# Performance work log

Measured on AMD Instinct MI355X. Metric: run time of the kernel, lower is better.

## Reference

```python
import jax, jax.numpy as jnp
import numpy as np

D_MODEL = 256
NUM_HEADS = 8
HEAD_DIM = D_MODEL // NUM_HEADS


def setup_inputs() -> dict:
    key = jax.random.key(0)
    ks = jax.random.split(key, 16)
    B, C, H, W = 2, D_MODEL, 64, 64
    s = 0.02
    inp = {
        "query_feat": jax.random.normal(ks[0], (B, C, H, W), jnp.float32),
        "lateral_feat": jax.random.normal(ks[1], (B, C, H, W), jnp.float32),
        # 1x1 convs == per-pixel linear layers: weight (out, in), bias (out,)
        "Wq": jax.random.normal(ks[2], (C, C), jnp.float32) * s,
        "bq": jnp.zeros((C,), jnp.float32),
        "Wk": jax.random.normal(ks[3], (C, C), jnp.float32) * s,
        "bk": jnp.zeros((C,), jnp.float32),
        "Wv": jax.random.normal(ks[4], (C, C), jnp.float32) * s,
        "bv": jnp.zeros((C,), jnp.float32),
        "Wo": jax.random.normal(ks[5], (C, C), jnp.float32) * s,
        "bo": jnp.zeros((C,), jnp.float32),
        "W1": jax.random.normal(ks[6], (4 * C, C), jnp.float32) * s,
        "b1": jnp.zeros((4 * C,), jnp.float32),
        "W2": jax.random.normal(ks[7], (C, 4 * C), jnp.float32) * s,
        "b2": jnp.zeros((C,), jnp.float32),
    }
    return inp


def reference(query_feat, lateral_feat, Wq, bq, Wk, bk, Wv, bv, Wo, bo, W1, b1, W2, b2):
    B, C, H, W = query_feat.shape
    N = H * W
    h, d = NUM_HEADS, HEAD_DIM
    scale = d ** -0.5

    # (B,C,H,W) -> (B,N,C) tokens
    xq = query_feat.reshape(B, C, N).transpose(0, 2, 1)
    xl = lateral_feat.reshape(B, C, N).transpose(0, 2, 1)

    # 1x1-conv projections = dense per-token linear
    Q = (xq @ Wq.T + bq).reshape(B, N, h, d).transpose(0, 2, 1, 3)  # (B,h,N,d)
    K = (xl @ Wk.T + bk).reshape(B, N, h, d).transpose(0, 2, 1, 3)
    V = (xl @ Wv.T + bv).reshape(B, N, h, d).transpose(0, 2, 1, 3)

    scores = jnp.einsum("bhqd,bhkd->bhqk", Q, K) * scale  # (B,h,N,N)
    attn = jax.nn.softmax(scores, axis=-1)  # dropout = identity at inference
    out = jnp.einsum("bhqk,bhkd->bhqd", attn, V)  # (B,h,N,d)

    out = out.transpose(0, 2, 1, 3).reshape(B, N, C)  # (B,N,C)
    out = out @ Wo.T + bo
    out = out.transpose(0, 2, 1).reshape(B, C, H, W)
    out = out + query_feat  # residual

    # MLP on channels (1x1 convs + exact GELU)
    t = out.reshape(B, C, N).transpose(0, 2, 1)  # (B,N,C)
    hdn = jax.nn.gelu(t @ W1.T + b1, approximate=False)  # (B,N,4C)
    mlp = (hdn @ W2.T + b2).transpose(0, 2, 1).reshape(B, C, H, W)
    return out + mlp
```

## Files before the change

### kernel.cpp

```cpp
#include <hip/hip_runtime.h>
#include <math.h>

namespace {

constexpr int kB  = 2;
constexpr int kC  = 256;
constexpr int kN  = 4096;
constexpr int kHD = 32;
constexpr int kC4 = 1024;

typedef __attribute__((ext_vector_type(8))) short bf16x8;
typedef __attribute__((ext_vector_type(4))) float f32x4;
typedef __attribute__((ext_vector_type(16))) float f32x16;

__device__ __forceinline__ float gelu_exact(float x) {
  return 0.5f * x * (1.0f + erff(x * 0.70710678118654752f));
}

__device__ __forceinline__ unsigned short f2bf(float x) {
  unsigned u = __builtin_bit_cast(unsigned, x);
  u += 0x7FFFu + ((u >> 16) & 1u);
  return (unsigned short)(u >> 16);
}

__device__ __forceinline__ float exp2_hw(float x) {
#if __has_builtin(__builtin_amdgcn_exp2f)
  return __builtin_amdgcn_exp2f(x);
#else
  float r;
  asm("v_exp_f32 %0, %1\n\ts_nop 1" : "=v"(r) : "v"(x));
  return r;
#endif
}

__device__ __forceinline__ unsigned cvt_pk_bf16(float lo, float hi) {
  unsigned r;
  asm("v_cvt_pk_bf16_f32 %0, %1, %2" : "=v"(r) : "v"(lo), "v"(hi));
  return r;
}

__global__ __launch_bounds__(256)
void convert_xpose(const float* __restrict__ qfeat, const float* __restrict__ lfeat,
                   unsigned short* __restrict__ qtok, unsigned short* __restrict__ ltok)
{
  __shared__ float Lds[32][36];
  const int z = blockIdx.z;
  const float* src = (z < kB) ? qfeat : lfeat;
  unsigned short* dst = (z < kB) ? qtok : ltok;
  const int b = z & 1;
  src += (size_t)b * kC * kN;
  dst += (size_t)b * kN * kC;
  const int n0 = blockIdx.x * 32, c0 = blockIdx.y * 32;
  const int t = threadIdx.x;
  const int r = t >> 3, q4 = (t & 7) * 4;
  {
    const float4 v = *(const float4*)&src[(size_t)(c0 + r) * kN + n0 + q4];
    Lds[r][q4 + 0] = v.x; Lds[r][q4 + 1] = v.y; Lds[r][q4 + 2] = v.z; Lds[r][q4 + 3] = v.w;
  }
  __syncthreads();
  ushort4 p;
  p.x = f2bf(Lds[q4 + 0][r]); p.y = f2bf(Lds[q4 + 1][r]);
  p.z = f2bf(Lds[q4 + 2][r]); p.w = f2bf(Lds[q4 + 3][r]);
  *(ushort4*)&dst[(size_t)(n0 + r) * kC + c0 + q4] = p;
}

__global__ __launch_bounds__(256)
void convert_w(const float* __restrict__ Wq, const float* __restrict__ Wk,
               const float* __restrict__ Wv, const float* __restrict__ Wo,
               const float* __restrict__ W1, const float* __restrict__ W2,
               unsigned short* __restrict__ dst)
{
  const int i4 = (blockIdx.x * 256 + threadIdx.x) * 4;
  const float* s; int base;
  if      (i4 < 65536)  { s = Wq; base = 0; }
  else if (i4 < 131072) { s = Wk; base = 65536; }
  else if (i4 < 196608) { s = Wv; base = 131072; }
  else if (i4 < 262144) { s = Wo; base = 196608; }
  else if (i4 < 524288) { s = W1; base = 262144; }
  else                  { s = W2; base = 524288; }
  const float4 v = *(const float4*)&s[i4 - base];
  ushort4 p;
  p.x = f2bf(v.x); p.y = f2bf(v.y); p.z = f2bf(v.z); p.w = f2bf(v.w);
  *(ushort4*)&dst[i4] = p;
}

template <int EPI, bool GELU, bool RES>
__global__ __launch_bounds__(256)
void gemm_mfma(const unsigned short* __restrict__ Wbf,
               const unsigned short* __restrict__ Xtok,
               const float* __restrict__ bias, const float* __restrict__ res,
               void* __restrict__ Y1, void* __restrict__ Y2,
               int M, int Nn, int K, float oscale)
{
  __shared__ unsigned short Wlds[64 * 64];
  __shared__ unsigned short Xlds[64 * 64];

  const int z = blockIdx.z;
  Xtok += (size_t)z * Nn * K;

  const int t = threadIdx.x;
  const int w = t >> 6, l = t & 63;
  const int r = l & 15, g = l >> 4;
  const int wm = w >> 1, wn = w & 1;
  const int m0 = blockIdx.y * 64, n0 = blockIdx.x * 64;

  const int rw = t >> 3;
  const int sw = (t & 7) ^ (rw & 7);
  const unsigned short* wsrc = Wbf + (size_t)(m0 + rw) * K + sw * 8;
  const unsigned short* xsrc = Xtok + (size_t)(n0 + rw) * K + sw * 8;

  f32x4 acc[2][2];
#pragma unroll
  for (int i = 0; i < 2; ++i)
#pragma unroll
    for (int j = 0; j < 2; ++j) acc[i][j] = {0.f, 0.f, 0.f, 0.f};

  bf16x8 wrg[2], xrg[2];
#pragma unroll
  for (int j = 0; j < 2; ++j) {
    wrg[j] = *(const bf16x8*)(wsrc + (size_t)(32 * j) * K);
    xrg[j] = *(const bf16x8*)(xsrc + (size_t)(32 * j) * K);
  }

  for (int k0 = 0; k0 < K; k0 += 64) {
    __syncthreads();
    *(bf16x8*)((char*)Wlds + t * 16)         = wrg[0];
    *(bf16x8*)((char*)Wlds + (256 + t) * 16) = wrg[1];
    *(bf16x8*)((char*)Xlds + t * 16)         = xrg[0];
    *(bf16x8*)((char*)Xlds + (256 + t) * 16) = xrg[1];
    __syncthreads();
    if (k0 + 64 < K) {
#pragma unroll
      for (int j = 0; j < 2; ++j) {
        wrg[j] = *(const bf16x8*)(wsrc + (size_t)(32 * j) * K + k0 + 64);
        xrg[j] = *(const bf16x8*)(xsrc + (size_t)(32 * j) * K + k0 + 64);
      }
    }
#pragma unroll
    for (int kc = 0; kc < 2; ++kc) {
      const int sl = ((kc * 4 + g) ^ (r & 7)) * 16;
      bf16x8 a0 = *(const bf16x8*)((const char*)Wlds + (wm * 32 + r) * 128 + sl);
      bf16x8 a1 = *(const bf16x8*)((const char*)Wlds + (wm * 32 + 16 + r) * 128 + sl);
      bf16x8 b0 = *(const bf16x8*)((const char*)Xlds + (wn * 32 + r) * 128 + sl);
      bf16x8 b1 = *(const bf16x8*)((const char*)Xlds + (wn * 32 + 16 + r) * 128 + sl);
      acc[0][0] = __builtin_amdgcn_mfma_f32_16x16x32_bf16(a0, b0, acc[0][0], 0, 0, 0);
      acc[0][1] = __builtin_amdgcn_mfma_f32_16x16x32_bf16(a0, b1, acc[0][1], 0, 0, 0);
      acc[1][0] = __builtin_amdgcn_mfma_f32_16x16x32_bf16(a1, b0, acc[1][0], 0, 0, 0);
      acc[1][1] = __builtin_amdgcn_mfma_f32_16x16x32_bf16(a1, b1, acc[1][1], 0, 0, 0);
    }
  }

#pragma unroll
  for (int f = 0; f < 2; ++f) {
    const int mb = m0 + wm * 32 + f * 16 + 4 * g;
    const float* bp = bias + mb;
    if constexpr (EPI == 4) { if (mb >= (M >> 1)) bp = res + (mb - (M >> 1)); }
    const float4 b4 = *(const float4*)bp;
#pragma unroll
    for (int fn = 0; fn < 2; ++fn) {
      const int n = n0 + wn * 32 + fn * 16 + r;
      float v[4];
      v[0] = (acc[f][fn][0] + b4.x) * oscale; v[1] = (acc[f][fn][1] + b4.y) * oscale;
      v[2] = (acc[f][fn][2] + b4.z) * oscale; v[3] = (acc[f][fn][3] + b4.w) * oscale;
      if (GELU) {
#pragma unroll
        for (int q = 0; q < 4; ++q) v[q] = gelu_exact(v[q]);
      }
      if (RES) {
#pragma unroll
        for (int q = 0; q < 4; ++q)
          v[q] += res[(size_t)z * M * Nn + (size_t)(mb + q) * Nn + n];
      }
      if constexpr (EPI == 0 || EPI == 3) {
        float* Yf = (float*)Y1 + (size_t)z * M * Nn;
#pragma unroll
        for (int q = 0; q < 4; ++q) Yf[(size_t)(mb + q) * Nn + n] = v[q];
      }
      if constexpr (EPI == 1 || EPI == 3) {
        unsigned short* Yt = (unsigned short*)((EPI == 3) ? Y2 : Y1) + (size_t)z * Nn * M;
        ushort4 pk;
        pk.x = f2bf(v[0]); pk.y = f2bf(v[1]); pk.z = f2bf(v[2]); pk.w = f2bf(v[3]);
        *(ushort4*)&Yt[(size_t)n * M + mb] = pk;
      }
      if constexpr (EPI == 4) {
        const int Mh = M >> 1;
        if (mb < Mh) {
          unsigned short* Yt = (unsigned short*)Y1 + (size_t)z * Nn * Mh;
          ushort4 pk;
          pk.x = f2bf(v[0]); pk.y = f2bf(v[1]); pk.z = f2bf(v[2]); pk.w = f2bf(v[3]);
          *(ushort4*)&Yt[(size_t)n * Mh + mb] = pk;
        } else {
          unsigned short* Yc = (unsigned short*)Y2 + (size_t)z * Mh * Nn;
#pragma unroll
          for (int q = 0; q < 4; ++q) Yc[(size_t)(mb - Mh + q) * Nn + n] = f2bf(v[q]);
        }
      }
    }
  }
}

__global__ __launch_bounds__(512, 4)
void attn_mfma32(const unsigned short* __restrict__ Qbf,
                 const unsigned short* __restrict__ Kbf,
                 const unsigned short* __restrict__ Vbf,
                 unsigned short* __restrict__ Aout)
{
  __shared__ unsigned short Klds[2][2048];
  __shared__ unsigned short Vlds[2][2048];
  __shared__ float Scr[4][64][17];

  const int id = blockIdx.x;
  const int bh = id & 15;
  const int b = bh >> 3, hd = bh & 7;
  const int t = threadIdx.x;
  const int w = t >> 6, l = t & 63;
  const int r = l & 31, hi = l >> 5;
  const int qg = w >> 1, kh = w & 1;

  const unsigned short* Qb = Qbf + (size_t)b * kN * kC;
  const unsigned short* Kb = Kbf + (size_t)b * kN * kC;
  const unsigned short* Vb = Vbf + ((size_t)b * kC + hd * kHD) * kN;
  unsigned short* Ap = Aout + (size_t)b * kN * kC;

  const int q0 = (id >> 4) * 128 + qg * 32;

  const bf16x8 qf0 = *(const bf16x8*)&Qb[(size_t)(q0 + r) * kC + hd * kHD + hi * 8];
  const bf16x8 qf1 = *(const bf16x8*)&Qb[(size_t)(q0 + r) * kC + hd * kHD + 16 + hi * 8];

  const int tt = t & 255, th = t >> 8;
  const unsigned short* ksrc = Kb + (size_t)(th * 2048 + (tt >> 2)) * kC + hd * kHD + (tt & 3) * 8;
  const unsigned short* vsrc = Vb + (size_t)(tt >> 3) * kN + th * 2048 + (tt & 7) * 8;
  char* kdst = (char*)&Klds[th][0] + ((tt & 3) * 64 + ((tt >> 2) ^ (9 * (tt & 3)))) * 16;
  char* vdst = (char*)&Vlds[th][0] + ((tt & 7) * 32 + ((tt >> 3) ^ (tt & 7))) * 16;

  const int kb0 = kh * 4096;
  int koff[2][2], voff[2][2];
#pragma unroll
  for (int ds = 0; ds < 2; ++ds)
#pragma unroll
    for (int tile = 0; tile < 2; ++tile) {
      const int c = 2 * ds + hi;
      koff[ds][tile] = kb0 + (c * 64 + tile * 32 + (r ^ (9 * c))) * 16;
    }
#pragma unroll
  for (int ktile = 0; ktile < 2; ++ktile)
#pragma unroll
    for (int kc = 0; kc < 2; ++kc) {
      const int c = ktile * 4 + kc * 2 + hi;
      voff[ktile][kc] = kb0 + (c * 32 + (r ^ c)) * 16;
    }

  const f32x16 ZV = {0.f};
  f32x16 oA = ZV, oB = ZV;
  float lsum = 0.f;

  bf16x8 krg = *(const bf16x8*)ksrc;
  bf16x8 vrg = *(const bf16x8*)vsrc;

  for (int kt = 0; kt < 2048; kt += 64) {
    __syncthreads();
    *(bf16x8*)kdst = krg;
    *(bf16x8*)vdst = vrg;
    __syncthreads();
    if (kt + 64 < 2048) {
      krg = *(const bf16x8*)(ksrc + (size_t)(kt + 64) * kC);
      vrg = *(const bf16x8*)(vsrc + kt + 64);
    }

    bf16x8 ka00 = *(const bf16x8*)((const char*)Klds + koff[0][0]);
    bf16x8 ka10 = *(const bf16x8*)((const char*)Klds + koff[1][0]);
    bf16x8 ka01 = *(const bf16x8*)((const char*)Klds + koff[0][1]);
    bf16x8 ka11 = *(const bf16x8*)((const char*)Klds + koff[1][1]);
    __builtin_amdgcn_s_setprio(1);
    f32x16 s0 = __builtin_amdgcn_mfma_f32_32x32x16_bf16(ka00, qf0, ZV, 0, 0, 0);
    s0        = __builtin_amdgcn_mfma_f32_32x32x16_bf16(ka10, qf1, s0, 0, 0, 0);
    f32x16 s1 = __builtin_amdgcn_mfma_f32_32x32x16_bf16(ka01, qf0, ZV, 0, 0, 0);
    s1        = __builtin_amdgcn_mfma_f32_32x32x16_bf16(ka11, qf1, s1, 0, 0, 0);
    __builtin_amdgcn_s_setprio(0);

#pragma unroll
    for (int ktile = 0; ktile < 2; ++ktile) {
      const f32x16& sv = ktile ? s1 : s0;
      float pe[16];
#pragma unroll
      for (int j = 0; j < 16; ++j) pe[j] = exp2_hw(sv[j]);
      lsum += (((pe[0] + pe[1]) + (pe[2] + pe[3])) + ((pe[4] + pe[5]) + (pe[6] + pe[7])))
            + (((pe[8] + pe[9]) + (pe[10] + pe[11])) + ((pe[12] + pe[13]) + (pe[14] + pe[15])));
      const unsigned c0 = cvt_pk_bf16(pe[0], pe[1]),   c1 = cvt_pk_bf16(pe[2], pe[3]);
      const unsigned c2 = cvt_pk_bf16(pe[4], pe[5]),   c3 = cvt_pk_bf16(pe[6], pe[7]);
      const unsigned c4 = cvt_pk_bf16(pe[8], pe[9]),   c5 = cvt_pk_bf16(pe[10], pe[11]);
      const unsigned c6 = cvt_pk_bf16(pe[12], pe[13]), c7 = cvt_pk_bf16(pe[14], pe[15]);
      auto a02 = __builtin_amdgcn_permlane32_swap(c0, c2, false, false);
      auto a13 = __builtin_amdgcn_permlane32_swap(c1, c3, false, false);
      auto a46 = __builtin_amdgcn_permlane32_swap(c4, c6, false, false);
      auto a57 = __builtin_amdgcn_permlane32_swap(c5, c7, false, false);
      union { unsigned u[4]; bf16x8 v; } p0, p1;
      p0.u[0] = a02[0]; p0.u[1] = a13[0]; p0.u[2] = a02[1]; p0.u[3] = a13[1];
      p1.u[0] = a46[0]; p1.u[1] = a57[0]; p1.u[2] = a46[1]; p1.u[3] = a57[1];
      bf16x8 vf0 = *(const bf16x8*)((const char*)Vlds + voff[ktile][0]);
      bf16x8 vf1 = *(const bf16x8*)((const char*)Vlds + voff[ktile][1]);
      __builtin_amdgcn_s_setprio(1);
      oA = __builtin_amdgcn_mfma_f32_32x32x16_bf16(vf0, p0.v, oA, 0, 0, 0);
      oB = __builtin_amdgcn_mfma_f32_32x32x16_bf16(vf1, p1.v, oB, 0, 0, 0);
      __builtin_amdgcn_s_setprio(0);
    }
  }

  {
    auto pr = __builtin_amdgcn_permlane32_swap(
        __builtin_bit_cast(unsigned, lsum), __builtin_bit_cast(unsigned, lsum), false, false);
    lsum = __builtin_bit_cast(float, (unsigned)pr[0]) + __builtin_bit_cast(float, (unsigned)pr[1]);
  }
  float oS[16];
#pragma unroll
  for (int j = 0; j < 16; ++j) oS[j] = oA[j] + oB[j];

  if (kh == 1) {
    float* S = &Scr[qg][l][0];
#pragma unroll
    for (int j = 0; j < 16; ++j) S[j] = oS[j];
    S[16] = lsum;
  }
  __syncthreads();
  if (kh == 0) {
    const float* S = &Scr[qg][l][0];
#pragma unroll
    for (int j = 0; j < 16; ++j) oS[j] += S[j];
    lsum += S[16];
    const float inv = 1.f / lsum;

    unsigned* T = (unsigned*)&Scr[qg][0][0];
#pragma unroll
    for (int p = 0; p < 8; ++p) {
      const int r2 = 4 * (p >> 1) + 2 * hi + (p & 1);
      T[r2 * 33 + r] = cvt_pk_bf16(oS[2 * p] * inv, oS[2 * p + 1] * inv);
    }
    unsigned v[8];
#pragma unroll
    for (int j = 0; j < 8; ++j) v[j] = T[(8 * hi + j) * 33 + r];
    unsigned short* outp = Ap + (size_t)(q0 + r) * kC + hd * kHD + hi * 16;
    uint4 w0{v[0], v[1], v[2], v[3]}, w1{v[4], v[5], v[6], v[7]};
    *(uint4*)outp = w0;
    *(uint4*)(outp + 8) = w1;
  }
}

}

extern "C" void kernel_launch(void* const* d_in, const int* in_sizes, int n_in,
                              void* d_out, int out_size, void* d_ws, size_t ws_size,
                              hipStream_t stream)
{
  const float* qfeat = (const float*)d_in[0];
  const float* lfeat = (const float*)d_in[1];
  const float* Wq = (const float*)d_in[2];
  const float* bq = (const float*)d_in[3];
  const float* Wk = (const float*)d_in[4];
  const float* bk = (const float*)d_in[5];
  const float* Wv = (const float*)d_in[6];
  const float* bv = (const float*)d_in[7];
  const float* Wo = (const float*)d_in[8];
  const float* bo = (const float*)d_in[9];
  const float* W1 = (const float*)d_in[10];
  const float* b1 = (const float*)d_in[11];
  const float* W2 = (const float*)d_in[12];
  const float* b2 = (const float*)d_in[13];
  float* out = (float*)d_out;
  (void)in_sizes; (void)n_in; (void)out_size; (void)ws_size;

  constexpr float kScaleLog2e = 0.25506970f;

  const size_t bcn = (size_t)kB * kC * kN;
  unsigned short* qtok   = (unsigned short*)d_ws;
  unsigned short* ltok   = qtok + bcn;
  unsigned short* wbf    = ltok + bcn;
  unsigned short* qbf    = wbf + 786432;
  unsigned short* kbf    = qbf + bcn;
  unsigned short* vbf    = kbf + bcn;
  unsigned short* atok   = vbf + bcn;
  unsigned short* owstok = atok + bcn;
  unsigned short* h1tok  = owstok + bcn;
  float*          ows    = (float*)(h1tok + (size_t)kB * kC4 * kN);

  dim3 blk(256);

  convert_w<<<dim3(768), blk, 0, stream>>>(Wq, Wk, Wv, Wo, W1, W2, wbf);
  convert_xpose<<<dim3(kN / 32, kC / 32, 2 * kB), blk, 0, stream>>>(qfeat, lfeat, qtok, ltok);

  gemm_mfma<1, false, false><<<dim3(64, 4, 2), blk, 0, stream>>>(
      wbf, qtok, bq, nullptr, qbf, nullptr, kC, kN, kC, kScaleLog2e);
  gemm_mfma<4, false, false><<<dim3(64, 8, 2), blk, 0, stream>>>(
      wbf + 65536, ltok, bk, bv, kbf, vbf, 2 * kC, kN, kC, 1.0f);

  attn_mfma32<<<dim3(512), dim3(512), 0, stream>>>(qbf, kbf, vbf, atok);

  gemm_mfma<3, false, true><<<dim3(64, 4, 2), blk, 0, stream>>>(
      wbf + 196608, atok, bo, qfeat, ows, owstok, kC, kN, kC, 1.0f);
  gemm_mfma<1, true, false><<<dim3(64, 16, 2), blk, 0, stream>>>(
      wbf + 262144, owstok, b1, nullptr, h1tok, nullptr, kC4, kN, kC, 1.0f);
  gemm_mfma<0, false, true><<<dim3(64, 4, 2), blk, 0, stream>>>(
      wbf + 524288, h1tok, b2, ows, out, nullptr, kC, kN, kC4, 1.0f);
}
```

Measured before the change: 107.4 us.

## Merge conversion kernels, split attention keys four ways, drop fp32 residual buffer

Fuses the weight and activation conversion kernels into one launch. The attention kernel now uses 64 queries per block with a four-way key split, which doubles the grid and uses a unified shared buffer for staging and reduction. The fp32 intermediate for the attention output plus residual is removed, and the final GEMM reads the bf16 token copy as its residual instead. This saves a launch and fp32 traffic, but the residual now carries bf16 rounding, and the larger key split adds reduction work.

```diff
diff --git a/kernel.cpp b/kernel.cpp
--- a/kernel.cpp
+++ b/kernel.cpp
@@ -21,6 +21,10 @@
   unsigned u = __builtin_bit_cast(unsigned, x);
   u += 0x7FFFu + ((u >> 16) & 1u);
   return (unsigned short)(u >> 16);
+}
+
+__device__ __forceinline__ float bf2f(unsigned short us) {
+  return __builtin_bit_cast(float, (unsigned)us << 16);
 }
 
 __device__ __forceinline__ float exp2_hw(float x) {
@@ -40,48 +44,49 @@
 }
 
 __global__ __launch_bounds__(256)
-void convert_xpose(const float* __restrict__ qfeat, const float* __restrict__ lfeat,
-                   unsigned short* __restrict__ qtok, unsigned short* __restrict__ ltok)
+void convert_all(const float* __restrict__ qfeat, const float* __restrict__ lfeat,
+                 const float* __restrict__ Wq, const float* __restrict__ Wk,
+                 const float* __restrict__ Wv, const float* __restrict__ Wo,
+                 const float* __restrict__ W1, const float* __restrict__ W2,
+                 unsigned short* __restrict__ qtok, unsigned short* __restrict__ ltok,
+                 unsigned short* __restrict__ wbf)
 {
   __shared__ float Lds[32][36];
   const int z = blockIdx.z;
-  const float* src = (z < kB) ? qfeat : lfeat;
-  unsigned short* dst = (z < kB) ? qtok : ltok;
-  const int b = z & 1;
-  src += (size_t)b * kC * kN;
-  dst += (size_t)b * kN * kC;
-  const int n0 = blockIdx.x * 32, c0 = blockIdx.y * 32;
   const int t = threadIdx.x;
-  const int r = t >> 3, q4 = (t & 7) * 4;
-  {
-    const float4 v = *(const float4*)&src[(size_t)(c0 + r) * kN + n0 + q4];
-    Lds[r][q4 + 0] = v.x; Lds[r][q4 + 1] = v.y; Lds[r][q4 + 2] = v.z; Lds[r][q4 + 3] = v.w;
-  }
-  __syncthreads();
-  ushort4 p;
-  p.x = f2bf(Lds[q4 + 0][r]); p.y = f2bf(Lds[q4 + 1][r]);
-  p.z = f2bf(Lds[q4 + 2][r]); p.w = f2bf(Lds[q4 + 3][r]);
-  *(ushort4*)&dst[(size_t)(n0 + r) * kC + c0 + q4] = p;
-}
-
-__global__ __launch_bounds__(256)
-void convert_w(const float* __restrict__ Wq, const float* __restrict__ Wk,
-               const float* __restrict__ Wv, const float* __restrict__ Wo,
-               const float* __restrict__ W1, const float* __restrict__ W2,
-               unsigned short* __restrict__ dst)
-{
-  const int i4 = (blockIdx.x * 256 + threadIdx.x) * 4;
-  const float* s; int base;
-  if      (i4 < 65536)  { s = Wq; base = 0; }
-  else if (i4 < 131072) { s = Wk; base = 65536; }
-  else if (i4 < 196608) { s = Wv; base = 131072; }
-  else if (i4 < 262144) { s = Wo; base = 196608; }
-  else if (i4 < 524288) { s = W1; base = 262144; }
-  else                  { s = W2; base = 524288; }
-  const float4 v = *(const float4*)&s[i4 - base];
-  ushort4 p;
-  p.x = f2bf(v.x); p.y = f2bf(v.y); p.z = f2bf(v.z); p.w = f2bf(v.w);
-  *(ushort4*)&dst[i4] = p;
+  if (z < 4) {
+    const float* src = (z < kB) ? qfeat : lfeat;
+    unsigned short* dst = (z < kB) ? qtok : ltok;
+    const int b = z & 1;
+    src += (size_t)b * kC * kN;
+    dst += (size_t)b * kN * kC;
+    const int n0 = blockIdx.x * 32, c0 = blockIdx.y * 32;
+    const int r = t >> 3, q4 = (t & 7) * 4;
+    {
+      const float4 v = *(const float4*)&src[(size_t)(c0 + r) * kN + n0 + q4];
+      Lds[r][q4 + 0] = v.x; Lds[r][q4 + 1] = v.y; Lds[r][q4 + 2] = v.z; Lds[r][q4 + 3] = v.w;
+    }
+    __syncthreads();
+    ushort4 p;
+    p.x = f2bf(Lds[q4 + 0][r]); p.y = f2bf(Lds[q4 + 1][r]);
+    p.z = f2bf(Lds[q4 + 2][r]); p.w = f2bf(Lds[q4 + 3][r]);
+    *(ushort4*)&dst[(size_t)(n0 + r) * kC + c0 + q4] = p;
+  } else {
+    const int wi = blockIdx.y * 128 + blockIdx.x;
+    if (wi >= 768) return;
+    const int i4 = wi * 1024 + t * 4;
+    const float* s; int base;
+    if      (i4 < 65536)  { s = Wq; base = 0; }
+    else if (i4 < 131072) { s = Wk; base = 65536; }
+    else if (i4 < 196608) { s = Wv; base = 131072; }
+    else if (i4 < 262144) { s = Wo; base = 196608; }
+    else if (i4 < 524288) { s = W1; base = 262144; }
+    else                  { s = W2; base = 524288; }
+    const float4 v = *(const float4*)&s[i4 - base];
+    ushort4 p;
+    p.x = f2bf(v.x); p.y = f2bf(v.y); p.z = f2bf(v.z); p.w = f2bf(v.w);
+    *(ushort4*)&wbf[i4] = p;
+  }
 }
 
 template <int EPI, bool GELU, bool RES>
@@ -171,13 +176,8 @@
         for (int q = 0; q < 4; ++q)
           v[q] += res[(size_t)z * M * Nn + (size_t)(mb + q) * Nn + n];
       }
-      if constexpr (EPI == 0 || EPI == 3) {
-        float* Yf = (float*)Y1 + (size_t)z * M * Nn;
-#pragma unroll
-        for (int q = 0; q < 4; ++q) Yf[(size_t)(mb + q) * Nn + n] = v[q];
-      }
-      if constexpr (EPI == 1 || EPI == 3) {
-        unsigned short* Yt = (unsigned short*)((EPI == 3) ? Y2 : Y1) + (size_t)z * Nn * M;
+      if constexpr (EPI == 1) {
+        unsigned short* Yt = (unsigned short*)Y1 + (size_t)z * Nn * M;
         ushort4 pk;
         pk.x = f2bf(v[0]); pk.y = f2bf(v[1]); pk.z = f2bf(v[2]); pk.w = f2bf(v[3]);
         *(ushort4*)&Yt[(size_t)n * M + mb] = pk;
@@ -195,6 +195,13 @@
           for (int q = 0; q < 4; ++q) Yc[(size_t)(mb - Mh + q) * Nn + n] = f2bf(v[q]);
         }
       }
+      if constexpr (EPI == 6) {
+        float* Yf = (float*)Y1 + (size_t)z * M * Nn;
+        const unsigned short* Rt = (const unsigned short*)Y2 + (size_t)z * Nn * M;
+#pragma unroll
+        for (int q = 0; q < 4; ++q)
+          Yf[(size_t)(mb + q) * Nn + n] = v[q] + bf2f(Rt[(size_t)n * M + mb + q]);
+      }
     }
   }
 }
@@ -205,9 +212,7 @@
                  const unsigned short* __restrict__ Vbf,
                  unsigned short* __restrict__ Aout)
 {
-  __shared__ unsigned short Klds[2][2048];
-  __shared__ unsigned short Vlds[2][2048];
-  __shared__ float Scr[4][64][17];
+  __shared__ char smem[32768];
 
   const int id = blockIdx.x;
   const int bh = id & 15;
@@ -215,25 +220,29 @@
   const int t = threadIdx.x;
   const int w = t >> 6, l = t & 63;
   const int r = l & 31, hi = l >> 5;
-  const int qg = w >> 1, kh = w & 1;
+  const int qg = w >> 2, kh = w & 3;
 
   const unsigned short* Qb = Qbf + (size_t)b * kN * kC;
   const unsigned short* Kb = Kbf + (size_t)b * kN * kC;
   const unsigned short* Vb = Vbf + ((size_t)b * kC + hd * kHD) * kN;
   unsigned short* Ap = Aout + (size_t)b * kN * kC;
 
-  const int q0 = (id >> 4) * 128 + qg * 32;
+  const int q0 = (id >> 4) * 64 + qg * 32;
 
   const bf16x8 qf0 = *(const bf16x8*)&Qb[(size_t)(q0 + r) * kC + hd * kHD + hi * 8];
   const bf16x8 qf1 = *(const bf16x8*)&Qb[(size_t)(q0 + r) * kC + hd * kHD + 16 + hi * 8];
 
-  const int tt = t & 255, th = t >> 8;
-  const unsigned short* ksrc = Kb + (size_t)(th * 2048 + (tt >> 2)) * kC + hd * kHD + (tt & 3) * 8;
-  const unsigned short* vsrc = Vb + (size_t)(tt >> 3) * kN + th * 2048 + (tt & 7) * 8;
-  char* kdst = (char*)&Klds[th][0] + ((tt & 3) * 64 + ((tt >> 2) ^ (9 * (tt & 3)))) * 16;
-  char* vdst = (char*)&Vlds[th][0] + ((tt & 7) * 32 + ((tt >> 3) ^ (tt & 7))) * 16;
-
-  const int kb0 = kh * 4096;
+  const int tq = t & 127, qd = t >> 7;
+  const int skey = tq >> 1, schalf = (tq & 1) * 2;
+  const int sd = tq >> 2, scp = (tq & 3) * 2;
+  const unsigned short* ksrc = Kb + (size_t)(qd * 1024 + skey) * kC + hd * kHD + schalf * 8;
+  const unsigned short* vsrc = Vb + (size_t)sd * kN + qd * 1024 + scp * 8;
+  char* kdst0 = smem + qd * 8192 + ((schalf)*64 + (skey ^ (9 * schalf))) * 16;
+  char* kdst1 = smem + qd * 8192 + ((schalf + 1) * 64 + (skey ^ (9 * (schalf + 1)))) * 16;
+  char* vdst0 = smem + qd * 8192 + 4096 + ((scp)*32 + (sd ^ scp)) * 16;
+  char* vdst1 = smem + qd * 8192 + 4096 + ((scp + 1) * 32 + (sd ^ (scp + 1))) * 16;
+
+  const int kb0 = kh * 8192;
   int koff[2][2], voff[2][2];
 #pragma unroll
   for (int ds = 0; ds < 2; ++ds)
@@ -247,30 +256,31 @@
 #pragma unroll
     for (int kc = 0; kc < 2; ++kc) {
       const int c = ktile * 4 + kc * 2 + hi;
-      voff[ktile][kc] = kb0 + (c * 32 + (r ^ c)) * 16;
+      voff[ktile][kc] = kb0 + 4096 + (c * 32 + (r ^ c)) * 16;
     }
 
   const f32x16 ZV = {0.f};
   f32x16 oA = ZV, oB = ZV;
   float lsum = 0.f;
 
-  bf16x8 krg = *(const bf16x8*)ksrc;
-  bf16x8 vrg = *(const bf16x8*)vsrc;
-
-  for (int kt = 0; kt < 2048; kt += 64) {
+  bf16x8 krg0 = *(const bf16x8*)ksrc, krg1 = *(const bf16x8*)(ksrc + 8);
+  bf16x8 vrg0 = *(const bf16x8*)vsrc, vrg1 = *(const bf16x8*)(vsrc + 8);
+
+  for (int it = 0; it < 16; ++it) {
     __syncthreads();
-    *(bf16x8*)kdst = krg;
-    *(bf16x8*)vdst = vrg;
+    *(bf16x8*)kdst0 = krg0; *(bf16x8*)kdst1 = krg1;
+    *(bf16x8*)vdst0 = vrg0; *(bf16x8*)vdst1 = vrg1;
     __syncthreads();
-    if (kt + 64 < 2048) {
-      krg = *(const bf16x8*)(ksrc + (size_t)(kt + 64) * kC);
-      vrg = *(const bf16x8*)(vsrc + kt + 64);
-    }
-
-    bf16x8 ka00 = *(const bf16x8*)((const char*)Klds + koff[0][0]);
-    bf16x8 ka10 = *(const bf16x8*)((const char*)Klds + koff[1][0]);
-    bf16x8 ka01 = *(const bf16x8*)((const char*)Klds + koff[0][1]);
-    bf16x8 ka11 = *(const bf16x8*)((const char*)Klds + koff[1][1]);
+    if (it + 1 < 16) {
+      ksrc += (size_t)64 * kC; vsrc += 64;
+      krg0 = *(const bf16x8*)ksrc; krg1 = *(const bf16x8*)(ksrc + 8);
+      vrg0 = *(const bf16x8*)vsrc; vrg1 = *(const bf16x8*)(vsrc + 8);
+    }
+
+    bf16x8 ka00 = *(const bf16x8*)(smem + koff[0][0]);
+    bf16x8 ka10 = *(const bf16x8*)(smem + koff[1][0]);
+    bf16x8 ka01 = *(const bf16x8*)(smem + koff[0][1]);
+    bf16x8 ka11 = *(const bf16x8*)(smem + koff[1][1]);
     __builtin_amdgcn_s_setprio(1);
     f32x16 s0 = __builtin_amdgcn_mfma_f32_32x32x16_bf16(ka00, qf0, ZV, 0, 0, 0);
     s0        = __builtin_amdgcn_mfma_f32_32x32x16_bf16(ka10, qf1, s0, 0, 0, 0);
@@ -297,8 +307,8 @@
       union { unsigned u[4]; bf16x8 v; } p0, p1;
       p0.u[0] = a02[0]; p0.u[1] = a13[0]; p0.u[2] = a02[1]; p0.u[3] = a13[1];
       p1.u[0] = a46[0]; p1.u[1] = a57[0]; p1.u[2] = a46[1]; p1.u[3] = a57[1];
-      bf16x8 vf0 = *(const bf16x8*)((const char*)Vlds + voff[ktile][0]);
-      bf16x8 vf1 = *(const bf16x8*)((const char*)Vlds + voff[ktile][1]);
+      bf16x8 vf0 = *(const bf16x8*)(smem + voff[ktile][0]);
+      bf16x8 vf1 = *(const bf16x8*)(smem + voff[ktile][1]);
       __builtin_amdgcn_s_setprio(1);
       oA = __builtin_amdgcn_mfma_f32_32x32x16_bf16(vf0, p0.v, oA, 0, 0, 0);
       oB = __builtin_amdgcn_mfma_f32_32x32x16_bf16(vf1, p1.v, oB, 0, 0, 0);
@@ -315,21 +325,26 @@
 #pragma unroll
   for (int j = 0; j < 16; ++j) oS[j] = oA[j] + oB[j];
 
-  if (kh == 1) {
-    float* S = &Scr[qg][l][0];
+  float* Scr = (float*)smem;
+  __syncthreads();
+  if (kh != 0) {
+    float* S = Scr + ((size_t)(qg * 3 + (kh - 1)) * 64 + l) * 17;
 #pragma unroll
     for (int j = 0; j < 16; ++j) S[j] = oS[j];
     S[16] = lsum;
   }
   __syncthreads();
   if (kh == 0) {
-    const float* S = &Scr[qg][l][0];
-#pragma unroll
-    for (int j = 0; j < 16; ++j) oS[j] += S[j];
-    lsum += S[16];
+#pragma unroll
+    for (int p = 0; p < 3; ++p) {
+      const float* S = Scr + ((size_t)(qg * 3 + p) * 64 + l) * 17;
+#pragma unroll
+      for (int j = 0; j < 16; ++j) oS[j] += S[j];
+      lsum += S[16];
+    }
     const float inv = 1.f / lsum;
 
-    unsigned* T = (unsigned*)&Scr[qg][0][0];
+    unsigned* T = (unsigned*)(Scr + (size_t)qg * 3 * 64 * 17);
 #pragma unroll
     for (int p = 0; p < 8; ++p) {
       const int r2 = 4 * (p >> 1) + 2 * hi + (p & 1);
@@ -380,24 +395,23 @@
   unsigned short* atok   = vbf + bcn;
   unsigned short* owstok = atok + bcn;
   unsigned short* h1tok  = owstok + bcn;
-  float*          ows    = (float*)(h1tok + (size_t)kB * kC4 * kN);
 
   dim3 blk(256);
 
-  convert_w<<<dim3(768), blk, 0, stream>>>(Wq, Wk, Wv, Wo, W1, W2, wbf);
-  convert_xpose<<<dim3(kN / 32, kC / 32, 2 * kB), blk, 0, stream>>>(qfeat, lfeat, qtok, ltok);
+  convert_all<<<dim3(128, 8, 5), blk, 0, stream>>>(
+      qfeat, lfeat, Wq, Wk, Wv, Wo, W1, W2, qtok, ltok, wbf);
 
   gemm_mfma<1, false, false><<<dim3(64, 4, 2), blk, 0, stream>>>(
       wbf, qtok, bq, nullptr, qbf, nullptr, kC, kN, kC, kScaleLog2e);
   gemm_mfma<4, false, false><<<dim3(64, 8, 2), blk, 0, stream>>>(
       wbf + 65536, ltok, bk, bv, kbf, vbf, 2 * kC, kN, kC, 1.0f);
 
-  attn_mfma32<<<dim3(512), dim3(512), 0, stream>>>(qbf, kbf, vbf, atok);
-
-  gemm_mfma<3, false, true><<<dim3(64, 4, 2), blk, 0, stream>>>(
-      wbf + 196608, atok, bo, qfeat, ows, owstok, kC, kN, kC, 1.0f);
+  attn_mfma32<<<dim3(1024), dim3(512), 0, stream>>>(qbf, kbf, vbf, atok);
+
+  gemm_mfma<1, false, true><<<dim3(64, 4, 2), blk, 0, stream>>>(
+      wbf + 196608, atok, bo, qfeat, owstok, nullptr, kC, kN, kC, 1.0f);
   gemm_mfma<1, true, false><<<dim3(64, 16, 2), blk, 0, stream>>>(
       wbf + 262144, owstok, b1, nullptr, h1tok, nullptr, kC4, kN, kC, 1.0f);
-  gemm_mfma<0, false, true><<<dim3(64, 4, 2), blk, 0, stream>>>(
-      wbf + 524288, h1tok, b2, ows, out, nullptr, kC, kN, kC4, 1.0f);
-}
+  gemm_mfma<6, false, false><<<dim3(64, 4, 2), blk, 0, stream>>>(
+      wbf + 524288, h1tok, b2, nullptr, out, owstok, kC, kN, kC4, 1.0f);
+}
```

Result: slower. 112.1 us (+4.3%).
